# Kernel optimization log

Hardware: AMD Instinct MI355X
Metric: run time of the kernel (lower is better)

The kernel has to match this reference:

```python
import jax, jax.numpy as jnp
import numpy as np


def setup_inputs() -> dict:
    key = jax.random.key(0)
    ks = jax.random.split(key, 4)
    b, n, d, dp = 8, 4096, 256, 512
    X = jax.random.normal(ks[0], (b, n, d), dtype=jnp.float32)
    P = jax.random.normal(ks[1], (b, n, d), dtype=jnp.float32)
    # linear hypernetwork params (Kaiming-ish scale)
    Wh1 = jax.random.normal(ks[2], (d, dp), dtype=jnp.float32) * (1.0 / np.sqrt(d))
    Wh2 = jax.random.normal(ks[3], (d, dp), dtype=jnp.float32) * (1.0 / np.sqrt(d))
    bh1 = jnp.zeros((dp,), dtype=jnp.float32)
    bh2 = jnp.zeros((dp,), dtype=jnp.float32)
    return {"X": X, "P": P, "Wh1": Wh1, "bh1": bh1, "Wh2": Wh2, "bh2": bh2}


def reference(X, P, Wh1, bh1, Wh2, bh2):
    # X, P: [b, n, d]
    Xp = X + P
    # hypernetwork-generated per-sample mixing weights: [b, n, d_prime]
    W1 = Xp @ Wh1 + bh1
    W2 = Xp @ Wh2 + bh2
    # token mixing: project tokens down to d_prime "mixing" space, GELU, back up
    Pm = jnp.einsum('bnp,bnd->bpd', W1, Xp)           # [b, d_prime, d]
    A = jax.nn.gelu(Pm, approximate=False)             # torch nn.GELU is exact erf form
    Y = jnp.einsum('bnp,bpd->bnd', W2, A)              # [b, n, d]
    return Y
```

## Files before the change

kernel.cpp:

```cpp
#include <hip/hip_runtime.h>

#define DEV static __device__ __forceinline__

typedef unsigned short u16;
typedef __bf16 bf16_t;
typedef __bf16 bf16x8 __attribute__((ext_vector_type(8)));
typedef float f32x4 __attribute__((ext_vector_type(4)));
typedef u16 u16x8 __attribute__((ext_vector_type(8)));

static constexpr int Bb = 8;
static constexpr int Nn = 4096;
static constexpr int Dd = 256;
static constexpr int DP = 512;

DEV void gload16(const void* g, void* l) {
  __builtin_amdgcn_global_load_lds(
      (__attribute__((address_space(1))) void*)(unsigned long long)(g),
      (__attribute__((address_space(3))) void*)(unsigned)(unsigned long long)(l),
      16, 0, 0);
}

DEV u16 f2bf(float x) { bf16_t h = (bf16_t)x; return __builtin_bit_cast(u16, h); }
DEV float bf2f(u16 v) { unsigned u = ((unsigned)v) << 16; return __builtin_bit_cast(float, u); }
DEV float gelu_exact(float x) { return 0.5f * x * (1.0f + erff(x * 0.70710678118654752f)); }

template <int NT>
DEV void gemm_tile(const u16* Ag, int lda, const u16* Bg, int ldb,
                   int k0, int ksteps, u16* ldsA, u16* ldsB, f32x4 acc[4][NT]) {
  constexpr int BCH  = NT / 2;
  constexpr int ABUF = 4096;
  constexpr int BBUF = NT * 1024;
  const int tid  = threadIdx.x;
  const int wave = tid >> 6, lane = tid & 63;
  const int wr = wave >> 1, wc = wave & 1;
  const int lr = lane & 15, lk = (lane >> 4) * 8;
  const int srow = lane >> 2;
  const int skb  = (lane & 3) * 8;
  const int ca0 = wave * 2, ca1 = ca0 + 1;
  const size_t ga0 = (size_t)(ca0 * 16 + srow) * lda + skb;
  const size_t ga1 = (size_t)(ca1 * 16 + srow) * lda + skb;
  u16* la0 = ldsA + ca0 * 512; u16* la1 = ldsA + ca1 * 512;
  size_t gb[BCH]; u16* lb[BCH];
#pragma unroll
  for (int i = 0; i < BCH; ++i) {
    const int ch = wave * BCH + i;
    gb[i] = (size_t)(ch * 16 + srow) * ldb + skb;
    lb[i] = ldsB + ch * 512;
  }

  auto STAGE = [&](int kt, int buf) {
    const int kk = k0 + kt * 32;
    gload16(Ag + ga0 + kk, la0 + buf * ABUF);
    gload16(Ag + ga1 + kk, la1 + buf * ABUF);
#pragma unroll
    for (int i = 0; i < BCH; ++i) gload16(Bg + gb[i] + kk, lb[i] + buf * BBUF);
  };

  STAGE(0, 0);
  STAGE(1, 1);
  if constexpr (NT == 2) asm volatile("s_waitcnt vmcnt(3)" ::: "memory");
  else                   asm volatile("s_waitcnt vmcnt(4)" ::: "memory");
  __builtin_amdgcn_s_barrier();
  __builtin_amdgcn_sched_barrier(0);

  int cur = 0;
  for (int kt = 0; kt < ksteps; ++kt) {
    const int sb = (cur + 2 >= 3) ? cur - 1 : cur + 2;
    const bool do_stage = (kt + 2 < ksteps);
    if (do_stage) STAGE(kt + 2, sb);
    const u16* pa = ldsA + cur * ABUF;
    const u16* pb = ldsB + cur * BBUF;
    bf16x8 af[4], bfr[NT];
#pragma unroll
    for (int m = 0; m < 4; ++m)
      af[m] = *(const bf16x8*)(pa + (wr * 64 + m * 16 + lr) * 32 + lk);
#pragma unroll
    for (int n = 0; n < NT; ++n)
      bfr[n] = *(const bf16x8*)(pb + (wc * (NT * 16) + n * 16 + lr) * 32 + lk);
#pragma unroll
    for (int m = 0; m < 4; ++m)
#pragma unroll
      for (int n = 0; n < NT; ++n)
        acc[m][n] = __builtin_amdgcn_mfma_f32_16x16x32_bf16(af[m], bfr[n], acc[m][n], 0, 0, 0);
    if (kt + 1 < ksteps) {
      if (do_stage) {
        if constexpr (NT == 2) asm volatile("s_waitcnt vmcnt(3)" ::: "memory");
        else                   asm volatile("s_waitcnt vmcnt(4)" ::: "memory");
      } else {
        asm volatile("s_waitcnt vmcnt(0)" ::: "memory");
      }
      __builtin_amdgcn_s_barrier();
      __builtin_amdgcn_sched_barrier(0);
    }
    cur = (cur + 1 == 3) ? 0 : cur + 1;
  }
  __builtin_amdgcn_s_barrier();
}

template <int NT>
DEV void acc_zero(f32x4 acc[4][NT]) {
#pragma unroll
  for (int m = 0; m < 4; ++m)
#pragma unroll
    for (int n = 0; n < NT; ++n) {
      f32x4 z = {0.f, 0.f, 0.f, 0.f};
      acc[m][n] = z;
    }
}

__global__ __launch_bounds__(256) void k_s1(const float* __restrict__ X, const float* __restrict__ P,
                                            const float* __restrict__ Wh1, const float* __restrict__ Wh2,
                                            u16* __restrict__ Xp, u16* __restrict__ XpT,
                                            float* __restrict__ s_part,
                                            u16* __restrict__ WhT1, u16* __restrict__ Wbf2) {
  __shared__ u16 lt[64 * 65];
  const int bid = blockIdx.x;
  const int t = threadIdx.x;
  if (bid < 2048) {
    const int b  = bid >> 8;
    const int nt = (bid >> 2) & 63;
    const int dt = bid & 3;
    const int n0 = nt * 64, d0 = dt * 64;
    const int r = t >> 2, c0 = (t & 3) * 16;
    const size_t gbase = ((size_t)(b * Nn + n0 + r)) * Dd + d0 + c0;
    u16x8 lo, hi;
#pragma unroll
    for (int i = 0; i < 4; ++i) {
      float4 xv = *(const float4*)(X + gbase + i * 4);
      float4 pv = *(const float4*)(P + gbase + i * 4);
      u16 a0 = f2bf(xv.x + pv.x), a1 = f2bf(xv.y + pv.y);
      u16 a2 = f2bf(xv.z + pv.z), a3 = f2bf(xv.w + pv.w);
      if (i < 2) { lo[i*4+0]=a0; lo[i*4+1]=a1; lo[i*4+2]=a2; lo[i*4+3]=a3; }
      else       { int q=(i-2)*4; hi[q+0]=a0; hi[q+1]=a1; hi[q+2]=a2; hi[q+3]=a3; }
      lt[r * 65 + c0 + i*4 + 0] = a0; lt[r * 65 + c0 + i*4 + 1] = a1;
      lt[r * 65 + c0 + i*4 + 2] = a2; lt[r * 65 + c0 + i*4 + 3] = a3;
    }
    *(u16x8*)(Xp + gbase)     = lo;
    *(u16x8*)(Xp + gbase + 8) = hi;
    __syncthreads();
    const int dd = t >> 2, nc0 = (t & 3) * 16;
    u16x8 olo, ohi;
    float colsum = 0.f;
#pragma unroll
    for (int i = 0; i < 8; ++i) { olo[i] = lt[(nc0 + i) * 65 + dd]; colsum += bf2f(olo[i]); }
#pragma unroll
    for (int i = 0; i < 8; ++i) { ohi[i] = lt[(nc0 + 8 + i) * 65 + dd]; colsum += bf2f(ohi[i]); }
    const size_t obase = ((size_t)(b * Dd + d0 + dd)) * Nn + n0 + nc0;
    *(u16x8*)(XpT + obase)     = olo;
    *(u16x8*)(XpT + obase + 8) = ohi;
    colsum += __shfl_xor(colsum, 1);
    colsum += __shfl_xor(colsum, 2);
    if ((t & 3) == 0) s_part[(size_t)(b * 64 + nt) * Dd + d0 + dd] = colsum;
  } else if (bid < 2048 + 32) {
    const int wb = bid - 2048;
    const int rt = (wb >> 3) & 3;
    const int ct = wb & 7;
    const int r0 = rt * 64, c0t = ct * 64;
    const int r = t >> 2, c0 = (t & 3) * 16;
    const size_t gbase = (size_t)(r0 + r) * DP + c0t + c0;
#pragma unroll
    for (int i = 0; i < 4; ++i) {
      float4 v = *(const float4*)(Wh1 + gbase + i * 4);
      lt[r * 65 + c0 + i*4 + 0] = f2bf(v.x); lt[r * 65 + c0 + i*4 + 1] = f2bf(v.y);
      lt[r * 65 + c0 + i*4 + 2] = f2bf(v.z); lt[r * 65 + c0 + i*4 + 3] = f2bf(v.w);
    }
    __syncthreads();
    const int pp = t >> 2, dc0 = (t & 3) * 16;
    u16x8 olo, ohi;
#pragma unroll
    for (int i = 0; i < 8; ++i) olo[i] = lt[(dc0 + i) * 65 + pp];
#pragma unroll
    for (int i = 0; i < 8; ++i) ohi[i] = lt[(dc0 + 8 + i) * 65 + pp];
    u16* out = WhT1 + (size_t)(c0t + pp) * Dd + r0 + dc0;
    *(u16x8*)(out)     = olo;
    *(u16x8*)(out + 8) = ohi;
  } else {
    const int idx = ((bid - 2048 - 32) * 256 + t) * 8;
    float4 v0 = *(const float4*)(Wh2 + idx);
    float4 v1 = *(const float4*)(Wh2 + idx + 4);
    u16x8 o;
    o[0]=f2bf(v0.x); o[1]=f2bf(v0.y); o[2]=f2bf(v0.z); o[3]=f2bf(v0.w);
    o[4]=f2bf(v1.x); o[5]=f2bf(v1.y); o[6]=f2bf(v1.z); o[7]=f2bf(v1.w);
    *(u16x8*)(Wbf2 + idx) = o;
  }
}

__global__ __launch_bounds__(256) void k_gram(const u16* __restrict__ XpT, u16* __restrict__ G_part) {
  __shared__ __align__(16) u16 ldsA[3 * 128 * 32];
  __shared__ __align__(16) u16 ldsB[3 * 64 * 32];
  const int bid0 = blockIdx.x;
  const int bid = (bid0 & 7) * 64 + (bid0 >> 3);
  const int kc = bid & 7;
  const int tn = (bid >> 3) & 3;
  const int tm = (bid >> 5) & 1;
  const int b  = bid >> 6;
  const u16* Ag = XpT + (size_t)(b * Dd + tm * 128) * Nn;
  const u16* Bg = XpT + (size_t)(b * Dd + tn * 64) * Nn;
  f32x4 acc[4][2];
  acc_zero<2>(acc);
  gemm_tile<2>(Ag, Nn, Bg, Nn, kc * 512, 16, ldsA, ldsB, acc);
  const int tid = threadIdx.x, wave = tid >> 6, lane = tid & 63;
  const int wr = wave >> 1, wc = wave & 1, lr = lane & 15, lq = lane >> 4;
  u16* base = G_part + (size_t)kc * (Bb * Dd * Dd) + (size_t)(b * Dd + tm * 128) * Dd + tn * 64;
#pragma unroll
  for (int m = 0; m < 4; ++m)
#pragma unroll
    for (int n = 0; n < 2; ++n)
#pragma unroll
      for (int j = 0; j < 4; ++j)
        base[(size_t)(wr * 64 + m * 16 + lq * 4 + j) * Dd + wc * 32 + n * 16 + lr] =
            f2bf(acc[m][n][j]);
}

__global__ __launch_bounds__(256) void k_gsum(const u16* __restrict__ G_part,
                                              const float* __restrict__ s_part,
                                              u16* __restrict__ Gb, float* __restrict__ s,
                                              float* __restrict__ c) {
  const int bid = blockIdx.x;
  const int t = threadIdx.x;
  if (bid < 8) {
    const int b = bid, d = t;
    float sum = 0.f;
#pragma unroll 8
    for (int nt = 0; nt < 64; ++nt) sum += s_part[(size_t)(b * 64 + nt) * Dd + d];
    s[b * Dd + d] = sum;
    c[b * Dd + d] = 0.f;
  } else {
    const int e = ((bid - 8) * 256 + t) * 8;
    float a[8] = {0.f,0.f,0.f,0.f,0.f,0.f,0.f,0.f};
#pragma unroll
    for (int k = 0; k < 8; ++k) {
      u16x8 v = *(const u16x8*)(G_part + (size_t)k * (Bb * Dd * Dd) + e);
#pragma unroll
      for (int i = 0; i < 8; ++i) a[i] += bf2f(v[i]);
    }
    u16x8 o;
#pragma unroll
    for (int i = 0; i < 8; ++i) o[i] = f2bf(a[i]);
    *(u16x8*)(Gb + e) = o;
  }
}

__global__ __launch_bounds__(256) void k_pmAT(const u16* __restrict__ WhT1, const u16* __restrict__ Gb,
                                              const float* __restrict__ bh1, const float* __restrict__ s,
                                              const float* __restrict__ bh2,
                                              u16* __restrict__ AT, float* __restrict__ c) {
  __shared__ __align__(16) u16 smem[24576];
  u16* ldsA = smem;
  u16* ldsB = smem + 12288;
  u16* ct   = smem;
  const int bid = blockIdx.x;
  const int tn = bid & 1;
  const int tm = (bid >> 1) & 3;
  const int b  = bid >> 3;
  const int p0 = tm * 128, d0 = tn * 128;
  const u16* Ag = WhT1 + (size_t)p0 * Dd;
  const u16* Bg = Gb + (size_t)(b * Dd + d0) * Dd;
  f32x4 acc[4][4];
  acc_zero<4>(acc);
  gemm_tile<4>(Ag, Dd, Bg, Dd, 0, Dd / 32, ldsA, ldsB, acc);
  const int tid = threadIdx.x, wave = tid >> 6, lane = tid & 63;
  const int wr = wave >> 1, wc = wave & 1, lr = lane & 15, lq = lane >> 4;
#pragma unroll
  for (int n = 0; n < 4; ++n) {
    const int col = wc * 64 + n * 16 + lr;
    const float sv = s[b * Dd + d0 + col];
#pragma unroll
    for (int m = 0; m < 4; ++m) {
#pragma unroll
      for (int j = 0; j < 4; ++j) {
        const int row = wr * 64 + m * 16 + lq * 4 + j;
        const float pm = acc[m][n][j] + bh1[p0 + row] * sv;
        ct[col * 136 + row] = f2bf(gelu_exact(pm));
      }
    }
  }
  __syncthreads();
#pragma unroll
  for (int it = 0; it < 8; ++it) {
    const int id = tid + it * 256;
    const int dl = id >> 4, ch = id & 15;
    *(u16x8*)(AT + (size_t)(b * Dd + d0 + dl) * DP + p0 + ch * 8) =
        *(const u16x8*)(ct + dl * 136 + ch * 8);
  }
  const int ccol = tid >> 1;
  const int chalf = tid & 1;
  float csum = 0.f;
#pragma unroll
  for (int q = 0; q < 8; ++q) {
    u16x8 av = *(const u16x8*)(ct + ccol * 136 + chalf * 64 + q * 8);
#pragma unroll
    for (int i = 0; i < 8; ++i) csum += bh2[p0 + chalf * 64 + q * 8 + i] * bf2f(av[i]);
  }
  csum += __shfl_xor(csum, 1);
  if (chalf == 0) atomicAdd(c + b * Dd + d0 + ccol, csum);
}

__global__ __launch_bounds__(256) void k_h(const u16* __restrict__ Wbf2, const u16* __restrict__ AT,
                                           u16* __restrict__ HT) {
  __shared__ __align__(16) u16 smem[24576];
  u16* ldsA = smem;
  u16* ldsB = smem + 12288;
  u16* ct   = smem;
  const int bid = blockIdx.x;
  const int tn = bid & 1;
  const int tm = (bid >> 1) & 1;
  const int b  = bid >> 2;
  const int k0 = tm * 128, d0 = tn * 128;
  const u16* Ag = Wbf2 + (size_t)k0 * DP;
  const u16* Bg = AT + (size_t)(b * Dd + d0) * DP;
  f32x4 acc[4][4];
  acc_zero<4>(acc);
  gemm_tile<4>(Ag, DP, Bg, DP, 0, DP / 32, ldsA, ldsB, acc);
  const int tid = threadIdx.x, wave = tid >> 6, lane = tid & 63;
  const int wr = wave >> 1, wc = wave & 1, lr = lane & 15, lq = lane >> 4;
#pragma unroll
  for (int n = 0; n < 4; ++n) {
    const int col = wc * 64 + n * 16 + lr;
#pragma unroll
    for (int m = 0; m < 4; ++m)
#pragma unroll
      for (int j = 0; j < 4; ++j)
        ct[col * 136 + wr * 64 + m * 16 + lq * 4 + j] = f2bf(acc[m][n][j]);
  }
  __syncthreads();
#pragma unroll
  for (int it = 0; it < 8; ++it) {
    const int id = tid + it * 256;
    const int dl = id >> 4, ch = id & 15;
    *(u16x8*)(HT + (size_t)(b * Dd + d0 + dl) * Dd + k0 + ch * 8) =
        *(const u16x8*)(ct + dl * 136 + ch * 8);
  }
}

__global__ __launch_bounds__(256) void k_y(const u16* __restrict__ Xp, const u16* __restrict__ HT,
                                           const float* __restrict__ c, float* __restrict__ Y) {
  __shared__ __align__(16) u16 ldsA[3 * 128 * 32];
  __shared__ __align__(16) u16 ldsB[3 * 64 * 32];
  const int bid0 = blockIdx.x;
  const int bid = (bid0 & 7) * 128 + (bid0 >> 3);
  const int b  = bid >> 7;
  const int tm = (bid >> 2) & 31;
  const int tn = bid & 3;
  const u16* Ag = Xp + (size_t)(b * Nn + tm * 128) * Dd;
  const u16* Bg = HT + (size_t)(b * Dd + tn * 64) * Dd;
  f32x4 acc[4][2];
  acc_zero<2>(acc);
  gemm_tile<2>(Ag, Dd, Bg, Dd, 0, Dd / 32, ldsA, ldsB, acc);
  const int tid = threadIdx.x, wave = tid >> 6, lane = tid & 63;
  const int wr = wave >> 1, wc = wave & 1, lr = lane & 15, lq = lane >> 4;
  float* base = Y + (size_t)(b * Nn + tm * 128) * Dd + tn * 64;
#pragma unroll
  for (int n = 0; n < 2; ++n) {
    const int col = wc * 32 + n * 16 + lr;
    const float cv = c[b * Dd + tn * 64 + col];
#pragma unroll
    for (int m = 0; m < 4; ++m)
#pragma unroll
      for (int j = 0; j < 4; ++j)
        base[(size_t)(wr * 64 + m * 16 + lq * 4 + j) * Dd + col] = acc[m][n][j] + cv;
  }
}

extern "C" void kernel_launch(void* const* d_in, const int* in_sizes, int n_in,
                              void* d_out, int out_size, void* d_ws, size_t ws_size,
                              hipStream_t stream) {
  const float* X   = (const float*)d_in[0];
  const float* P   = (const float*)d_in[1];
  const float* Wh1 = (const float*)d_in[2];
  const float* bh1 = (const float*)d_in[3];
  const float* Wh2 = (const float*)d_in[4];
  const float* bh2 = (const float*)d_in[5];
  float* Y = (float*)d_out;
  char* ws = (char*)d_ws;

  u16*   Xp     = (u16*)(ws);
  u16*   XpT    = (u16*)(ws + 16777216);
  u16*   WhT1   = (u16*)(ws + 33554432);
  u16*   Wbf2   = (u16*)(ws + 33816576);
  u16*   G_part = (u16*)(ws + 34078720);
  float* s_part = (float*)(ws + 42467328);
  float* s      = (float*)(ws + 42991616);
  float* c      = (float*)(ws + 42999808);
  u16*   Gb     = (u16*)(ws + 43008000);
  u16*   AT     = (u16*)(ws + 44056576);
  u16*   HT     = (u16*)(ws + 46153728);
  const size_t WS_NEED = 47202304;
  if (ws_size < WS_NEED) return;

  k_s1  <<<2144, 256, 0, stream>>>(X, P, Wh1, Wh2, Xp, XpT, s_part, WhT1, Wbf2);
  k_gram<<<512,  256, 0, stream>>>(XpT, G_part);
  k_gsum<<<264,  256, 0, stream>>>(G_part, s_part, Gb, s, c);
  k_pmAT<<<64,   256, 0, stream>>>(WhT1, Gb, bh1, s, bh2, AT, c);
  k_h   <<<32,   256, 0, stream>>>(Wbf2, AT, HT);
  k_y   <<<1024, 256, 0, stream>>>(Xp, HT, c, Y);
}
```

Baseline: 68.00 us.

## Fuse gram reduction, Pm/GELU, and H GEMM into one kernel with grid counter

Removes the separate k_gsum, k_pmAT and k_h launches. The split-K gram partials are now summed while loading the B operand of the Pm GEMM, and the H GEMM runs in the first 32 blocks once a global atomic counter shows all 64 blocks have written AT. The c bias is written as per-tile partials and summed in k_y, so the atomics on c and the zeroing of c are no longer needed. This saves launch gaps and a round trip through memory, but it relies on all 64 blocks being resident at once for the spin-wait, and the Pm loop now has only two LDS buffers with no prefetch overlap.

```diff
diff --git a/kernel.cpp b/kernel.cpp
--- a/kernel.cpp
+++ b/kernel.cpp
@@ -185,10 +185,12 @@
   }
 }
 
-__global__ __launch_bounds__(256) void k_gram(const u16* __restrict__ XpT, u16* __restrict__ G_part) {
+__global__ __launch_bounds__(256) void k_gram(const u16* __restrict__ XpT, u16* __restrict__ G_part,
+                                              int* __restrict__ ctr) {
   __shared__ __align__(16) u16 ldsA[3 * 128 * 32];
   __shared__ __align__(16) u16 ldsB[3 * 64 * 32];
   const int bid0 = blockIdx.x;
+  if (bid0 == 512) { if (threadIdx.x == 0) *ctr = 0; return; }
   const int bid = (bid0 & 7) * 64 + (bid0 >> 3);
   const int kc = bid & 7;
   const int tn = (bid >> 3) & 3;
@@ -212,129 +214,161 @@
             f2bf(acc[m][n][j]);
 }
 
-__global__ __launch_bounds__(256) void k_gsum(const u16* __restrict__ G_part,
-                                              const float* __restrict__ s_part,
-                                              u16* __restrict__ Gb, float* __restrict__ s,
-                                              float* __restrict__ c) {
+__global__ __launch_bounds__(256) void k_pmATh(
+    const u16* __restrict__ WhT1, const u16* __restrict__ G_part,
+    const float* __restrict__ s_part, const float* __restrict__ bh1,
+    const float* __restrict__ bh2, const u16* __restrict__ Wbf2,
+    u16* __restrict__ AT, float* __restrict__ c_part, u16* __restrict__ HT,
+    int* __restrict__ ctr) {
+  __shared__ __align__(16) u16 smem[24576];
+  __shared__ float sv[128];
   const int bid = blockIdx.x;
-  const int t = threadIdx.x;
-  if (bid < 8) {
-    const int b = bid, d = t;
-    float sum = 0.f;
+  const int tid = threadIdx.x;
+  const int wave = tid >> 6, lane = tid & 63;
+  const int wr = wave >> 1, wc = wave & 1, lr = lane & 15, lq = lane >> 4;
+  const int lk = lq * 8;
+
+  {
+    const int tnb = bid & 1;
+    const int tmb = (bid >> 1) & 3;
+    const int bb  = bid >> 3;
+    const int p0 = tmb * 128, d0 = tnb * 128;
+
+    if (tid < 128) {
+      float sum = 0.f;
 #pragma unroll 8
-    for (int nt = 0; nt < 64; ++nt) sum += s_part[(size_t)(b * 64 + nt) * Dd + d];
-    s[b * Dd + d] = sum;
-    c[b * Dd + d] = 0.f;
-  } else {
-    const int e = ((bid - 8) * 256 + t) * 8;
-    float a[8] = {0.f,0.f,0.f,0.f,0.f,0.f,0.f,0.f};
-#pragma unroll
-    for (int k = 0; k < 8; ++k) {
-      u16x8 v = *(const u16x8*)(G_part + (size_t)k * (Bb * Dd * Dd) + e);
-#pragma unroll
-      for (int i = 0; i < 8; ++i) a[i] += bf2f(v[i]);
-    }
-    u16x8 o;
-#pragma unroll
-    for (int i = 0; i < 8; ++i) o[i] = f2bf(a[i]);
-    *(u16x8*)(Gb + e) = o;
-  }
-}
-
-__global__ __launch_bounds__(256) void k_pmAT(const u16* __restrict__ WhT1, const u16* __restrict__ Gb,
-                                              const float* __restrict__ bh1, const float* __restrict__ s,
-                                              const float* __restrict__ bh2,
-                                              u16* __restrict__ AT, float* __restrict__ c) {
-  __shared__ __align__(16) u16 smem[24576];
-  u16* ldsA = smem;
-  u16* ldsB = smem + 12288;
-  u16* ct   = smem;
-  const int bid = blockIdx.x;
-  const int tn = bid & 1;
-  const int tm = (bid >> 1) & 3;
-  const int b  = bid >> 3;
-  const int p0 = tm * 128, d0 = tn * 128;
-  const u16* Ag = WhT1 + (size_t)p0 * Dd;
-  const u16* Bg = Gb + (size_t)(b * Dd + d0) * Dd;
-  f32x4 acc[4][4];
-  acc_zero<4>(acc);
-  gemm_tile<4>(Ag, Dd, Bg, Dd, 0, Dd / 32, ldsA, ldsB, acc);
-  const int tid = threadIdx.x, wave = tid >> 6, lane = tid & 63;
-  const int wr = wave >> 1, wc = wave & 1, lr = lane & 15, lq = lane >> 4;
-#pragma unroll
-  for (int n = 0; n < 4; ++n) {
-    const int col = wc * 64 + n * 16 + lr;
-    const float sv = s[b * Dd + d0 + col];
-#pragma unroll
-    for (int m = 0; m < 4; ++m) {
-#pragma unroll
-      for (int j = 0; j < 4; ++j) {
-        const int row = wr * 64 + m * 16 + lq * 4 + j;
-        const float pm = acc[m][n][j] + bh1[p0 + row] * sv;
-        ct[col * 136 + row] = f2bf(gelu_exact(pm));
+      for (int nt = 0; nt < 64; ++nt) sum += s_part[(size_t)(bb * 64 + nt) * Dd + d0 + tid];
+      sv[tid] = sum;
+    }
+
+    const u16* Ag = WhT1 + (size_t)p0 * Dd;
+    const int srow = lane >> 2, skb = (lane & 3) * 8;
+    const int ca0 = wave * 2, ca1 = ca0 + 1;
+    const size_t ga0 = (size_t)(ca0 * 16 + srow) * Dd + skb;
+    const size_t ga1 = (size_t)(ca1 * 16 + srow) * Dd + skb;
+    const int brow = tid >> 1, bhalf = tid & 1;
+    const u16* Bbase = G_part + (size_t)(bb * Dd + d0 + brow) * Dd + bhalf * 16;
+
+    f32x4 acc[4][4];
+    acc_zero<4>(acc);
+    for (int kt = 0; kt < 8; ++kt) {
+      const int buf = kt & 1;
+      u16* lA = smem + buf * 4096;
+      u16* lB = smem + 8192 + buf * 4096;
+      gload16(Ag + ga0 + kt * 32, lA + ca0 * 512);
+      gload16(Ag + ga1 + kt * 32, lA + ca1 * 512);
+      float a[16];
+#pragma unroll
+      for (int i = 0; i < 16; ++i) a[i] = 0.f;
+#pragma unroll
+      for (int sl = 0; sl < 8; ++sl) {
+        const u16* p = Bbase + (size_t)sl * (Bb * Dd * Dd) + kt * 32;
+        u16x8 v0 = *(const u16x8*)p;
+        u16x8 v1 = *(const u16x8*)(p + 8);
+#pragma unroll
+        for (int i = 0; i < 8; ++i) { a[i] += bf2f(v0[i]); a[8 + i] += bf2f(v1[i]); }
       }
-    }
-  }
+      u16x8 o0, o1;
+#pragma unroll
+      for (int i = 0; i < 8; ++i) { o0[i] = f2bf(a[i]); o1[i] = f2bf(a[8 + i]); }
+      *(u16x8*)(lB + brow * 32 + bhalf * 16)     = o0;
+      *(u16x8*)(lB + brow * 32 + bhalf * 16 + 8) = o1;
+      asm volatile("s_waitcnt vmcnt(0)" ::: "memory");
+      __syncthreads();
+      bf16x8 af[4], bfr[4];
+#pragma unroll
+      for (int m = 0; m < 4; ++m)
+        af[m] = *(const bf16x8*)(lA + (wr * 64 + m * 16 + lr) * 32 + lk);
+#pragma unroll
+      for (int n = 0; n < 4; ++n)
+        bfr[n] = *(const bf16x8*)(lB + (wc * 64 + n * 16 + lr) * 32 + lk);
+#pragma unroll
+      for (int m = 0; m < 4; ++m)
+#pragma unroll
+        for (int n = 0; n < 4; ++n)
+          acc[m][n] = __builtin_amdgcn_mfma_f32_16x16x32_bf16(af[m], bfr[n], acc[m][n], 0, 0, 0);
+      __syncthreads();
+    }
+
+    u16* ct = smem;
+#pragma unroll
+    for (int n = 0; n < 4; ++n) {
+      const int col = wc * 64 + n * 16 + lr;
+      const float svv = sv[col];
+#pragma unroll
+      for (int m = 0; m < 4; ++m) {
+#pragma unroll
+        for (int j = 0; j < 4; ++j) {
+          const int row = wr * 64 + m * 16 + lq * 4 + j;
+          const float pm = acc[m][n][j] + bh1[p0 + row] * svv;
+          ct[col * 136 + row] = f2bf(gelu_exact(pm));
+        }
+      }
+    }
+    __syncthreads();
+#pragma unroll
+    for (int it = 0; it < 8; ++it) {
+      const int id = tid + it * 256;
+      const int dl = id >> 4, ch = id & 15;
+      *(u16x8*)(AT + (size_t)(bb * Dd + d0 + dl) * DP + p0 + ch * 8) =
+          *(const u16x8*)(ct + dl * 136 + ch * 8);
+    }
+    const int ccol = tid >> 1;
+    const int chalf = tid & 1;
+    float csum = 0.f;
+#pragma unroll
+    for (int q = 0; q < 8; ++q) {
+      u16x8 av = *(const u16x8*)(ct + ccol * 136 + chalf * 64 + q * 8);
+#pragma unroll
+      for (int i = 0; i < 8; ++i) csum += bh2[p0 + chalf * 64 + q * 8 + i] * bf2f(av[i]);
+    }
+    csum += __shfl_xor(csum, 1);
+    if (chalf == 0) c_part[(size_t)(bb * 4 + tmb) * Dd + d0 + ccol] = csum;
+  }
+
+  __threadfence();
   __syncthreads();
-#pragma unroll
-  for (int it = 0; it < 8; ++it) {
-    const int id = tid + it * 256;
-    const int dl = id >> 4, ch = id & 15;
-    *(u16x8*)(AT + (size_t)(b * Dd + d0 + dl) * DP + p0 + ch * 8) =
-        *(const u16x8*)(ct + dl * 136 + ch * 8);
-  }
-  const int ccol = tid >> 1;
-  const int chalf = tid & 1;
-  float csum = 0.f;
-#pragma unroll
-  for (int q = 0; q < 8; ++q) {
-    u16x8 av = *(const u16x8*)(ct + ccol * 136 + chalf * 64 + q * 8);
-#pragma unroll
-    for (int i = 0; i < 8; ++i) csum += bh2[p0 + chalf * 64 + q * 8 + i] * bf2f(av[i]);
-  }
-  csum += __shfl_xor(csum, 1);
-  if (chalf == 0) atomicAdd(c + b * Dd + d0 + ccol, csum);
-}
-
-__global__ __launch_bounds__(256) void k_h(const u16* __restrict__ Wbf2, const u16* __restrict__ AT,
-                                           u16* __restrict__ HT) {
-  __shared__ __align__(16) u16 smem[24576];
-  u16* ldsA = smem;
-  u16* ldsB = smem + 12288;
-  u16* ct   = smem;
-  const int bid = blockIdx.x;
-  const int tn = bid & 1;
-  const int tm = (bid >> 1) & 1;
-  const int b  = bid >> 2;
-  const int k0 = tm * 128, d0 = tn * 128;
-  const u16* Ag = Wbf2 + (size_t)k0 * DP;
-  const u16* Bg = AT + (size_t)(b * Dd + d0) * DP;
-  f32x4 acc[4][4];
-  acc_zero<4>(acc);
-  gemm_tile<4>(Ag, DP, Bg, DP, 0, DP / 32, ldsA, ldsB, acc);
-  const int tid = threadIdx.x, wave = tid >> 6, lane = tid & 63;
-  const int wr = wave >> 1, wc = wave & 1, lr = lane & 15, lq = lane >> 4;
-#pragma unroll
-  for (int n = 0; n < 4; ++n) {
-    const int col = wc * 64 + n * 16 + lr;
-#pragma unroll
-    for (int m = 0; m < 4; ++m)
-#pragma unroll
-      for (int j = 0; j < 4; ++j)
-        ct[col * 136 + wr * 64 + m * 16 + lq * 4 + j] = f2bf(acc[m][n][j]);
+  if (tid == 0) atomicAdd(ctr, 1);
+  if (bid >= 32) return;
+  if (tid == 0) {
+    while (atomicAdd(ctr, 0) < 64) __builtin_amdgcn_s_sleep(8);
   }
   __syncthreads();
-#pragma unroll
-  for (int it = 0; it < 8; ++it) {
-    const int id = tid + it * 256;
-    const int dl = id >> 4, ch = id & 15;
-    *(u16x8*)(HT + (size_t)(b * Dd + d0 + dl) * Dd + k0 + ch * 8) =
-        *(const u16x8*)(ct + dl * 136 + ch * 8);
+  __threadfence();
+
+  {
+    const int tn = bid & 1;
+    const int tm = (bid >> 1) & 1;
+    const int b  = bid >> 2;
+    const int k0 = tm * 128, d0 = tn * 128;
+    const u16* Ag = Wbf2 + (size_t)k0 * DP;
+    const u16* Bg = AT + (size_t)(b * Dd + d0) * DP;
+    f32x4 acc[4][4];
+    acc_zero<4>(acc);
+    gemm_tile<4>(Ag, DP, Bg, DP, 0, DP / 32, smem, smem + 12288, acc);
+    u16* ct = smem;
+#pragma unroll
+    for (int n = 0; n < 4; ++n) {
+      const int col = wc * 64 + n * 16 + lr;
+#pragma unroll
+      for (int m = 0; m < 4; ++m)
+#pragma unroll
+        for (int j = 0; j < 4; ++j)
+          ct[col * 136 + wr * 64 + m * 16 + lq * 4 + j] = f2bf(acc[m][n][j]);
+    }
+    __syncthreads();
+#pragma unroll
+    for (int it = 0; it < 8; ++it) {
+      const int id = tid + it * 256;
+      const int dl = id >> 4, ch = id & 15;
+      *(u16x8*)(HT + (size_t)(b * Dd + d0 + dl) * Dd + k0 + ch * 8) =
+          *(const u16x8*)(ct + dl * 136 + ch * 8);
+    }
   }
 }
 
 __global__ __launch_bounds__(256) void k_y(const u16* __restrict__ Xp, const u16* __restrict__ HT,
-                                           const float* __restrict__ c, float* __restrict__ Y) {
+                                           const float* __restrict__ c_part, float* __restrict__ Y) {
   __shared__ __align__(16) u16 ldsA[3 * 128 * 32];
   __shared__ __align__(16) u16 ldsB[3 * 64 * 32];
   const int bid0 = blockIdx.x;
@@ -353,7 +387,9 @@
 #pragma unroll
   for (int n = 0; n < 2; ++n) {
     const int col = wc * 32 + n * 16 + lr;
-    const float cv = c[b * Dd + tn * 64 + col];
+    const int gcol = tn * 64 + col;
+    float cv = c_part[(size_t)(b * 4 + 0) * Dd + gcol] + c_part[(size_t)(b * 4 + 1) * Dd + gcol]
+             + c_part[(size_t)(b * 4 + 2) * Dd + gcol] + c_part[(size_t)(b * 4 + 3) * Dd + gcol];
 #pragma unroll
     for (int m = 0; m < 4; ++m)
 #pragma unroll
@@ -380,18 +416,15 @@
   u16*   Wbf2   = (u16*)(ws + 33816576);
   u16*   G_part = (u16*)(ws + 34078720);
   float* s_part = (float*)(ws + 42467328);
-  float* s      = (float*)(ws + 42991616);
-  float* c      = (float*)(ws + 42999808);
-  u16*   Gb     = (u16*)(ws + 43008000);
-  u16*   AT     = (u16*)(ws + 44056576);
-  u16*   HT     = (u16*)(ws + 46153728);
-  const size_t WS_NEED = 47202304;
+  float* c_part = (float*)(ws + 42991616);
+  int*   ctr    = (int*)(ws + 43024384);
+  u16*   AT     = (u16*)(ws + 43024512);
+  u16*   HT     = (u16*)(ws + 45121664);
+  const size_t WS_NEED = 46170240;
   if (ws_size < WS_NEED) return;
 
-  k_s1  <<<2144, 256, 0, stream>>>(X, P, Wh1, Wh2, Xp, XpT, s_part, WhT1, Wbf2);
-  k_gram<<<512,  256, 0, stream>>>(XpT, G_part);
-  k_gsum<<<264,  256, 0, stream>>>(G_part, s_part, Gb, s, c);
-  k_pmAT<<<64,   256, 0, stream>>>(WhT1, Gb, bh1, s, bh2, AT, c);
-  k_h   <<<32,   256, 0, stream>>>(Wbf2, AT, HT);
-  k_y   <<<1024, 256, 0, stream>>>(Xp, HT, c, Y);
-}
+  k_s1   <<<2144, 256, 0, stream>>>(X, P, Wh1, Wh2, Xp, XpT, s_part, WhT1, Wbf2);
+  k_gram <<<513,  256, 0, stream>>>(XpT, G_part, ctr);
+  k_pmATh<<<64,   256, 0, stream>>>(WhT1, G_part, s_part, bh1, bh2, Wbf2, AT, c_part, HT, ctr);
+  k_y    <<<1024, 256, 0, stream>>>(Xp, HT, c_part, Y);
+}
```

After: 85.29 us. 25.4% more time.

## Fuse GELU mixing-matrix kernel with H projection, keeping activations in LDS

Applied to the files above, without the earlier changes.

Merges k_pmAT and k_h into one kernel. Each block loops over the four d_prime tiles, computes the GELU activation tile into shared memory, and immediately accumulates the Wh2 product into registers. This removes the AT round-trip through global memory, one kernel launch, and the atomic accumulation of c, since c is now written directly. In exchange the grid shrinks from 64 to 32 blocks, the first GEMM is recomputed by both km blocks, and the inner H loop is serialized with synchronous loads and no prefetch.

```diff
diff --git a/kernel.cpp b/kernel.cpp
--- a/kernel.cpp
+++ b/kernel.cpp
@@ -214,8 +214,7 @@
 
 __global__ __launch_bounds__(256) void k_gsum(const u16* __restrict__ G_part,
                                               const float* __restrict__ s_part,
-                                              u16* __restrict__ Gb, float* __restrict__ s,
-                                              float* __restrict__ c) {
+                                              u16* __restrict__ Gb, float* __restrict__ s) {
   const int bid = blockIdx.x;
   const int t = threadIdx.x;
   if (bid < 8) {
@@ -224,7 +223,6 @@
 #pragma unroll 8
     for (int nt = 0; nt < 64; ++nt) sum += s_part[(size_t)(b * 64 + nt) * Dd + d];
     s[b * Dd + d] = sum;
-    c[b * Dd + d] = 0.f;
   } else {
     const int e = ((bid - 8) * 256 + t) * 8;
     float a[8] = {0.f,0.f,0.f,0.f,0.f,0.f,0.f,0.f};
@@ -241,87 +239,95 @@
   }
 }
 
-__global__ __launch_bounds__(256) void k_pmAT(const u16* __restrict__ WhT1, const u16* __restrict__ Gb,
-                                              const float* __restrict__ bh1, const float* __restrict__ s,
-                                              const float* __restrict__ bh2,
-                                              u16* __restrict__ AT, float* __restrict__ c) {
+__global__ __launch_bounds__(256) void k_pmATh(
+    const u16* __restrict__ WhT1, const u16* __restrict__ Gb,
+    const float* __restrict__ bh1, const float* __restrict__ s,
+    const float* __restrict__ bh2, const u16* __restrict__ Wbf2,
+    float* __restrict__ c, u16* __restrict__ HT) {
   __shared__ __align__(16) u16 smem[24576];
   u16* ldsA = smem;
   u16* ldsB = smem + 12288;
-  u16* ct   = smem;
+  u16* act  = smem;
+  u16* hA   = smem + 17920;
   const int bid = blockIdx.x;
-  const int tn = bid & 1;
-  const int tm = (bid >> 1) & 3;
-  const int b  = bid >> 3;
-  const int p0 = tm * 128, d0 = tn * 128;
-  const u16* Ag = WhT1 + (size_t)p0 * Dd;
-  const u16* Bg = Gb + (size_t)(b * Dd + d0) * Dd;
-  f32x4 acc[4][4];
-  acc_zero<4>(acc);
-  gemm_tile<4>(Ag, Dd, Bg, Dd, 0, Dd / 32, ldsA, ldsB, acc);
-  const int tid = threadIdx.x, wave = tid >> 6, lane = tid & 63;
+  const int km = bid & 1;
+  const int tn = (bid >> 1) & 1;
+  const int b  = bid >> 2;
+  const int d0 = tn * 128, k0 = km * 128;
+  const int tid = threadIdx.x;
+  const int wave = tid >> 6, lane = tid & 63;
   const int wr = wave >> 1, wc = wave & 1, lr = lane & 15, lq = lane >> 4;
+  const int lk = lq * 8;
+  const int srow = lane >> 2, skb = (lane & 3) * 8;
+  const int ca0 = wave * 2, ca1 = ca0 + 1;
+  const int ccol = tid >> 1, chalf = tid & 1;
+
+  f32x4 acch[4][4];
+  acc_zero<4>(acch);
+  float csum = 0.f;
+
+  for (int tm = 0; tm < 4; ++tm) {
+    const int p0 = tm * 128;
+    f32x4 accA[4][4];
+    acc_zero<4>(accA);
+    gemm_tile<4>(WhT1 + (size_t)p0 * Dd, Dd, Gb + (size_t)(b * Dd + d0) * Dd, Dd,
+                 0, Dd / 32, ldsA, ldsB, accA);
+#pragma unroll
+    for (int n = 0; n < 4; ++n) {
+      const int col = wc * 64 + n * 16 + lr;
+      const float sv = s[b * Dd + d0 + col];
+#pragma unroll
+      for (int m = 0; m < 4; ++m)
+#pragma unroll
+        for (int j = 0; j < 4; ++j) {
+          const int row = wr * 64 + m * 16 + lq * 4 + j;
+          act[col * 136 + row] = f2bf(gelu_exact(accA[m][n][j] + bh1[p0 + row] * sv));
+        }
+    }
+    __syncthreads();
+    if (km == 0) {
+#pragma unroll
+      for (int q = 0; q < 8; ++q) {
+        u16x8 av = *(const u16x8*)(act + ccol * 136 + chalf * 64 + q * 8);
+#pragma unroll
+        for (int i = 0; i < 8; ++i) csum += bh2[p0 + chalf * 64 + q * 8 + i] * bf2f(av[i]);
+      }
+    }
+    for (int kt = 0; kt < 4; ++kt) {
+      gload16(Wbf2 + (size_t)(k0 + ca0 * 16 + srow) * DP + p0 + kt * 32 + skb, hA + ca0 * 512);
+      gload16(Wbf2 + (size_t)(k0 + ca1 * 16 + srow) * DP + p0 + kt * 32 + skb, hA + ca1 * 512);
+      asm volatile("s_waitcnt vmcnt(0)" ::: "memory");
+      __syncthreads();
+      bf16x8 af[4], bfr[4];
+#pragma unroll
+      for (int m = 0; m < 4; ++m)
+        af[m] = *(const bf16x8*)(hA + (wr * 64 + m * 16 + lr) * 32 + lk);
+#pragma unroll
+      for (int n = 0; n < 4; ++n)
+        bfr[n] = *(const bf16x8*)(act + (wc * 64 + n * 16 + lr) * 136 + kt * 32 + lk);
+#pragma unroll
+      for (int m = 0; m < 4; ++m)
+#pragma unroll
+        for (int n = 0; n < 4; ++n)
+          acch[m][n] = __builtin_amdgcn_mfma_f32_16x16x32_bf16(af[m], bfr[n], acch[m][n], 0, 0, 0);
+      __syncthreads();
+    }
+  }
+
+  if (km == 0) {
+    csum += __shfl_xor(csum, 1);
+    if (chalf == 0) c[b * Dd + d0 + ccol] = csum;
+  }
+
+  u16* ct = smem;
 #pragma unroll
   for (int n = 0; n < 4; ++n) {
     const int col = wc * 64 + n * 16 + lr;
-    const float sv = s[b * Dd + d0 + col];
-#pragma unroll
-    for (int m = 0; m < 4; ++m) {
-#pragma unroll
-      for (int j = 0; j < 4; ++j) {
-        const int row = wr * 64 + m * 16 + lq * 4 + j;
-        const float pm = acc[m][n][j] + bh1[p0 + row] * sv;
-        ct[col * 136 + row] = f2bf(gelu_exact(pm));
-      }
-    }
-  }
-  __syncthreads();
-#pragma unroll
-  for (int it = 0; it < 8; ++it) {
-    const int id = tid + it * 256;
-    const int dl = id >> 4, ch = id & 15;
-    *(u16x8*)(AT + (size_t)(b * Dd + d0 + dl) * DP + p0 + ch * 8) =
-        *(const u16x8*)(ct + dl * 136 + ch * 8);
-  }
-  const int ccol = tid >> 1;
-  const int chalf = tid & 1;
-  float csum = 0.f;
-#pragma unroll
-  for (int q = 0; q < 8; ++q) {
-    u16x8 av = *(const u16x8*)(ct + ccol * 136 + chalf * 64 + q * 8);
-#pragma unroll
-    for (int i = 0; i < 8; ++i) csum += bh2[p0 + chalf * 64 + q * 8 + i] * bf2f(av[i]);
-  }
-  csum += __shfl_xor(csum, 1);
-  if (chalf == 0) atomicAdd(c + b * Dd + d0 + ccol, csum);
-}
-
-__global__ __launch_bounds__(256) void k_h(const u16* __restrict__ Wbf2, const u16* __restrict__ AT,
-                                           u16* __restrict__ HT) {
-  __shared__ __align__(16) u16 smem[24576];
-  u16* ldsA = smem;
-  u16* ldsB = smem + 12288;
-  u16* ct   = smem;
-  const int bid = blockIdx.x;
-  const int tn = bid & 1;
-  const int tm = (bid >> 1) & 1;
-  const int b  = bid >> 2;
-  const int k0 = tm * 128, d0 = tn * 128;
-  const u16* Ag = Wbf2 + (size_t)k0 * DP;
-  const u16* Bg = AT + (size_t)(b * Dd + d0) * DP;
-  f32x4 acc[4][4];
-  acc_zero<4>(acc);
-  gemm_tile<4>(Ag, DP, Bg, DP, 0, DP / 32, ldsA, ldsB, acc);
-  const int tid = threadIdx.x, wave = tid >> 6, lane = tid & 63;
-  const int wr = wave >> 1, wc = wave & 1, lr = lane & 15, lq = lane >> 4;
-#pragma unroll
-  for (int n = 0; n < 4; ++n) {
-    const int col = wc * 64 + n * 16 + lr;
 #pragma unroll
     for (int m = 0; m < 4; ++m)
 #pragma unroll
       for (int j = 0; j < 4; ++j)
-        ct[col * 136 + wr * 64 + m * 16 + lq * 4 + j] = f2bf(acc[m][n][j]);
+        ct[col * 136 + wr * 64 + m * 16 + lq * 4 + j] = f2bf(acch[m][n][j]);
   }
   __syncthreads();
 #pragma unroll
@@ -383,15 +389,13 @@
   float* s      = (float*)(ws + 42991616);
   float* c      = (float*)(ws + 42999808);
   u16*   Gb     = (u16*)(ws + 43008000);
-  u16*   AT     = (u16*)(ws + 44056576);
-  u16*   HT     = (u16*)(ws + 46153728);
-  const size_t WS_NEED = 47202304;
+  u16*   HT     = (u16*)(ws + 44056576);
+  const size_t WS_NEED = 45105152;
   if (ws_size < WS_NEED) return;
 
-  k_s1  <<<2144, 256, 0, stream>>>(X, P, Wh1, Wh2, Xp, XpT, s_part, WhT1, Wbf2);
-  k_gram<<<512,  256, 0, stream>>>(XpT, G_part);
-  k_gsum<<<264,  256, 0, stream>>>(G_part, s_part, Gb, s, c);
-  k_pmAT<<<64,   256, 0, stream>>>(WhT1, Gb, bh1, s, bh2, AT, c);
-  k_h   <<<32,   256, 0, stream>>>(Wbf2, AT, HT);
-  k_y   <<<1024, 256, 0, stream>>>(Xp, HT, c, Y);
-}
+  k_s1   <<<2144, 256, 0, stream>>>(X, P, Wh1, Wh2, Xp, XpT, s_part, WhT1, Wbf2);
+  k_gram <<<512,  256, 0, stream>>>(XpT, G_part);
+  k_gsum <<<264,  256, 0, stream>>>(G_part, s_part, Gb, s);
+  k_pmATh<<<32,   256, 0, stream>>>(WhT1, Gb, bh1, s, bh2, Wbf2, c, HT);
+  k_y    <<<1024, 256, 0, stream>>>(Xp, HT, c, Y);
+}
```

Result: slower. 101.4 us (+49.2%).

## Fuse split-K gram reduction into k_gram via last-block counters; halve pmAT/h tiles

Applied to the files above, without the earlier changes.

Removes the separate k_gsum launch. Each split-K gram tile group now bumps an atomic counter, and the last of its 8 blocks sums the bf16 partials into Gb. The s reduction moves into k_pmAT, and the atomic c accumulation becomes per-tile c_part partials that k_y sums. k_pmAT and k_h switch to 128x64 tiles, doubling their grid sizes to raise parallelism in those small stages. This saves one launch and adds fence/atomic overhead plus a serialized tail reduction in the last block of each group.

```diff
diff --git a/kernel.cpp b/kernel.cpp
--- a/kernel.cpp
+++ b/kernel.cpp
@@ -112,7 +112,8 @@
                                             const float* __restrict__ Wh1, const float* __restrict__ Wh2,
                                             u16* __restrict__ Xp, u16* __restrict__ XpT,
                                             float* __restrict__ s_part,
-                                            u16* __restrict__ WhT1, u16* __restrict__ Wbf2) {
+                                            u16* __restrict__ WhT1, u16* __restrict__ Wbf2,
+                                            int* __restrict__ ctr) {
   __shared__ u16 lt[64 * 65];
   const int bid = blockIdx.x;
   const int t = threadIdx.x;
@@ -174,7 +175,7 @@
     u16* out = WhT1 + (size_t)(c0t + pp) * Dd + r0 + dc0;
     *(u16x8*)(out)     = olo;
     *(u16x8*)(out + 8) = ohi;
-  } else {
+  } else if (bid < 2048 + 32 + 64) {
     const int idx = ((bid - 2048 - 32) * 256 + t) * 8;
     float4 v0 = *(const float4*)(Wh2 + idx);
     float4 v1 = *(const float4*)(Wh2 + idx + 4);
@@ -182,12 +183,16 @@
     o[0]=f2bf(v0.x); o[1]=f2bf(v0.y); o[2]=f2bf(v0.z); o[3]=f2bf(v0.w);
     o[4]=f2bf(v1.x); o[5]=f2bf(v1.y); o[6]=f2bf(v1.z); o[7]=f2bf(v1.w);
     *(u16x8*)(Wbf2 + idx) = o;
-  }
-}
-
-__global__ __launch_bounds__(256) void k_gram(const u16* __restrict__ XpT, u16* __restrict__ G_part) {
+  } else {
+    if (t < 64) ctr[t] = 0;
+  }
+}
+
+__global__ __launch_bounds__(256) void k_gram(const u16* __restrict__ XpT, u16* __restrict__ G_part,
+                                              u16* __restrict__ Gb, int* __restrict__ ctr) {
   __shared__ __align__(16) u16 ldsA[3 * 128 * 32];
   __shared__ __align__(16) u16 ldsB[3 * 64 * 32];
+  __shared__ int lastFlag;
   const int bid0 = blockIdx.x;
   const int bid = (bid0 & 7) * 64 + (bid0 >> 3);
   const int kc = bid & 7;
@@ -210,113 +215,118 @@
       for (int j = 0; j < 4; ++j)
         base[(size_t)(wr * 64 + m * 16 + lq * 4 + j) * Dd + wc * 32 + n * 16 + lr] =
             f2bf(acc[m][n][j]);
-}
-
-__global__ __launch_bounds__(256) void k_gsum(const u16* __restrict__ G_part,
+
+  __threadfence();
+  __syncthreads();
+  const int group = (b * 2 + tm) * 4 + tn;
+  if (tid == 0) lastFlag = (atomicAdd(&ctr[group], 1) == 7);
+  __syncthreads();
+  if (!lastFlag) return;
+  __threadfence();
+
+  const int r = tid >> 1, hf = tid & 1;
+  const size_t off = (size_t)(b * Dd + tm * 128 + r) * Dd + tn * 64 + hf * 32;
+  float a[32];
+#pragma unroll
+  for (int i = 0; i < 32; ++i) a[i] = 0.f;
+  for (int k = 0; k < 8; ++k) {
+    const u16* p = G_part + (size_t)k * (Bb * Dd * Dd) + off;
+#pragma unroll
+    for (int ch = 0; ch < 4; ++ch) {
+      u16x8 v = *(const u16x8*)(p + ch * 8);
+#pragma unroll
+      for (int i = 0; i < 8; ++i) a[ch * 8 + i] += bf2f(v[i]);
+    }
+  }
+#pragma unroll
+  for (int ch = 0; ch < 4; ++ch) {
+    u16x8 o;
+#pragma unroll
+    for (int i = 0; i < 8; ++i) o[i] = f2bf(a[ch * 8 + i]);
+    *(u16x8*)(Gb + off + ch * 8) = o;
+  }
+}
+
+__global__ __launch_bounds__(256) void k_pmAT(const u16* __restrict__ WhT1, const u16* __restrict__ Gb,
                                               const float* __restrict__ s_part,
-                                              u16* __restrict__ Gb, float* __restrict__ s,
-                                              float* __restrict__ c) {
+                                              const float* __restrict__ bh1, const float* __restrict__ bh2,
+                                              u16* __restrict__ AT, float* __restrict__ c_part) {
+  __shared__ __align__(16) u16 smem[18432];
+  __shared__ float sv[64];
   const int bid = blockIdx.x;
-  const int t = threadIdx.x;
-  if (bid < 8) {
-    const int b = bid, d = t;
+  const int tn = bid & 3;
+  const int tm = (bid >> 2) & 3;
+  const int b  = bid >> 4;
+  const int p0 = tm * 128, d0 = tn * 64;
+  const int tid = threadIdx.x;
+  if (tid < 64) {
     float sum = 0.f;
 #pragma unroll 8
-    for (int nt = 0; nt < 64; ++nt) sum += s_part[(size_t)(b * 64 + nt) * Dd + d];
-    s[b * Dd + d] = sum;
-    c[b * Dd + d] = 0.f;
-  } else {
-    const int e = ((bid - 8) * 256 + t) * 8;
-    float a[8] = {0.f,0.f,0.f,0.f,0.f,0.f,0.f,0.f};
-#pragma unroll
-    for (int k = 0; k < 8; ++k) {
-      u16x8 v = *(const u16x8*)(G_part + (size_t)k * (Bb * Dd * Dd) + e);
-#pragma unroll
-      for (int i = 0; i < 8; ++i) a[i] += bf2f(v[i]);
-    }
-    u16x8 o;
-#pragma unroll
-    for (int i = 0; i < 8; ++i) o[i] = f2bf(a[i]);
-    *(u16x8*)(Gb + e) = o;
-  }
-}
-
-__global__ __launch_bounds__(256) void k_pmAT(const u16* __restrict__ WhT1, const u16* __restrict__ Gb,
-                                              const float* __restrict__ bh1, const float* __restrict__ s,
-                                              const float* __restrict__ bh2,
-                                              u16* __restrict__ AT, float* __restrict__ c) {
-  __shared__ __align__(16) u16 smem[24576];
+    for (int nt = 0; nt < 64; ++nt) sum += s_part[(size_t)(b * 64 + nt) * Dd + d0 + tid];
+    sv[tid] = sum;
+  }
+  u16* ldsA = smem;
+  u16* ldsB = smem + 12288;
+  f32x4 acc[4][2];
+  acc_zero<2>(acc);
+  gemm_tile<2>(WhT1 + (size_t)p0 * Dd, Dd, Gb + (size_t)(b * Dd + d0) * Dd, Dd,
+               0, Dd / 32, ldsA, ldsB, acc);
+  const int wave = tid >> 6, lane = tid & 63;
+  const int wr = wave >> 1, wc = wave & 1, lr = lane & 15, lq = lane >> 4;
+  u16* ct = smem;
+#pragma unroll
+  for (int n = 0; n < 2; ++n) {
+    const int col = wc * 32 + n * 16 + lr;
+    const float svv = sv[col];
+#pragma unroll
+    for (int m = 0; m < 4; ++m)
+#pragma unroll
+      for (int j = 0; j < 4; ++j) {
+        const int row = wr * 64 + m * 16 + lq * 4 + j;
+        ct[col * 136 + row] = f2bf(gelu_exact(acc[m][n][j] + bh1[p0 + row] * svv));
+      }
+  }
+  __syncthreads();
+#pragma unroll
+  for (int it = 0; it < 4; ++it) {
+    const int id = tid + it * 256;
+    const int dl = id >> 4, ch = id & 15;
+    *(u16x8*)(AT + (size_t)(b * Dd + d0 + dl) * DP + p0 + ch * 8) =
+        *(const u16x8*)(ct + dl * 136 + ch * 8);
+  }
+  const int ccol = tid >> 2, qtr = tid & 3;
+  float csum = 0.f;
+#pragma unroll
+  for (int q = 0; q < 4; ++q) {
+    u16x8 av = *(const u16x8*)(ct + ccol * 136 + qtr * 32 + q * 8);
+#pragma unroll
+    for (int i = 0; i < 8; ++i) csum += bh2[p0 + qtr * 32 + q * 8 + i] * bf2f(av[i]);
+  }
+  csum += __shfl_xor(csum, 1);
+  csum += __shfl_xor(csum, 2);
+  if (qtr == 0) c_part[(size_t)(b * 4 + tm) * Dd + d0 + ccol] = csum;
+}
+
+__global__ __launch_bounds__(256) void k_h(const u16* __restrict__ Wbf2, const u16* __restrict__ AT,
+                                           u16* __restrict__ HT) {
+  __shared__ __align__(16) u16 smem[18432];
   u16* ldsA = smem;
   u16* ldsB = smem + 12288;
   u16* ct   = smem;
   const int bid = blockIdx.x;
-  const int tn = bid & 1;
-  const int tm = (bid >> 1) & 3;
+  const int tn = bid & 3;
+  const int tm = (bid >> 2) & 1;
   const int b  = bid >> 3;
-  const int p0 = tm * 128, d0 = tn * 128;
-  const u16* Ag = WhT1 + (size_t)p0 * Dd;
-  const u16* Bg = Gb + (size_t)(b * Dd + d0) * Dd;
-  f32x4 acc[4][4];
-  acc_zero<4>(acc);
-  gemm_tile<4>(Ag, Dd, Bg, Dd, 0, Dd / 32, ldsA, ldsB, acc);
+  const int k0 = tm * 128, d0 = tn * 64;
+  f32x4 acc[4][2];
+  acc_zero<2>(acc);
+  gemm_tile<2>(Wbf2 + (size_t)k0 * DP, DP, AT + (size_t)(b * Dd + d0) * DP, DP,
+               0, DP / 32, ldsA, ldsB, acc);
   const int tid = threadIdx.x, wave = tid >> 6, lane = tid & 63;
   const int wr = wave >> 1, wc = wave & 1, lr = lane & 15, lq = lane >> 4;
 #pragma unroll
-  for (int n = 0; n < 4; ++n) {
-    const int col = wc * 64 + n * 16 + lr;
-    const float sv = s[b * Dd + d0 + col];
-#pragma unroll
-    for (int m = 0; m < 4; ++m) {
-#pragma unroll
-      for (int j = 0; j < 4; ++j) {
-        const int row = wr * 64 + m * 16 + lq * 4 + j;
-        const float pm = acc[m][n][j] + bh1[p0 + row] * sv;
-        ct[col * 136 + row] = f2bf(gelu_exact(pm));
-      }
-    }
-  }
-  __syncthreads();
-#pragma unroll
-  for (int it = 0; it < 8; ++it) {
-    const int id = tid + it * 256;
-    const int dl = id >> 4, ch = id & 15;
-    *(u16x8*)(AT + (size_t)(b * Dd + d0 + dl) * DP + p0 + ch * 8) =
-        *(const u16x8*)(ct + dl * 136 + ch * 8);
-  }
-  const int ccol = tid >> 1;
-  const int chalf = tid & 1;
-  float csum = 0.f;
-#pragma unroll
-  for (int q = 0; q < 8; ++q) {
-    u16x8 av = *(const u16x8*)(ct + ccol * 136 + chalf * 64 + q * 8);
-#pragma unroll
-    for (int i = 0; i < 8; ++i) csum += bh2[p0 + chalf * 64 + q * 8 + i] * bf2f(av[i]);
-  }
-  csum += __shfl_xor(csum, 1);
-  if (chalf == 0) atomicAdd(c + b * Dd + d0 + ccol, csum);
-}
-
-__global__ __launch_bounds__(256) void k_h(const u16* __restrict__ Wbf2, const u16* __restrict__ AT,
-                                           u16* __restrict__ HT) {
-  __shared__ __align__(16) u16 smem[24576];
-  u16* ldsA = smem;
-  u16* ldsB = smem + 12288;
-  u16* ct   = smem;
-  const int bid = blockIdx.x;
-  const int tn = bid & 1;
-  const int tm = (bid >> 1) & 1;
-  const int b  = bid >> 2;
-  const int k0 = tm * 128, d0 = tn * 128;
-  const u16* Ag = Wbf2 + (size_t)k0 * DP;
-  const u16* Bg = AT + (size_t)(b * Dd + d0) * DP;
-  f32x4 acc[4][4];
-  acc_zero<4>(acc);
-  gemm_tile<4>(Ag, DP, Bg, DP, 0, DP / 32, ldsA, ldsB, acc);
-  const int tid = threadIdx.x, wave = tid >> 6, lane = tid & 63;
-  const int wr = wave >> 1, wc = wave & 1, lr = lane & 15, lq = lane >> 4;
-#pragma unroll
-  for (int n = 0; n < 4; ++n) {
-    const int col = wc * 64 + n * 16 + lr;
+  for (int n = 0; n < 2; ++n) {
+    const int col = wc * 32 + n * 16 + lr;
 #pragma unroll
     for (int m = 0; m < 4; ++m)
 #pragma unroll
@@ -325,7 +335,7 @@
   }
   __syncthreads();
 #pragma unroll
-  for (int it = 0; it < 8; ++it) {
+  for (int it = 0; it < 4; ++it) {
     const int id = tid + it * 256;
     const int dl = id >> 4, ch = id & 15;
     *(u16x8*)(HT + (size_t)(b * Dd + d0 + dl) * Dd + k0 + ch * 8) =
@@ -334,7 +344,7 @@
 }
 
 __global__ __launch_bounds__(256) void k_y(const u16* __restrict__ Xp, const u16* __restrict__ HT,
-                                           const float* __restrict__ c, float* __restrict__ Y) {
+                                           const float* __restrict__ c_part, float* __restrict__ Y) {
   __shared__ __align__(16) u16 ldsA[3 * 128 * 32];
   __shared__ __align__(16) u16 ldsB[3 * 64 * 32];
   const int bid0 = blockIdx.x;
@@ -353,7 +363,9 @@
 #pragma unroll
   for (int n = 0; n < 2; ++n) {
     const int col = wc * 32 + n * 16 + lr;
-    const float cv = c[b * Dd + tn * 64 + col];
+    const int gcol = tn * 64 + col;
+    const float cv = c_part[(size_t)(b * 4 + 0) * Dd + gcol] + c_part[(size_t)(b * 4 + 1) * Dd + gcol]
+                   + c_part[(size_t)(b * 4 + 2) * Dd + gcol] + c_part[(size_t)(b * 4 + 3) * Dd + gcol];
 #pragma unroll
     for (int m = 0; m < 4; ++m)
 #pragma unroll
@@ -380,18 +392,17 @@
   u16*   Wbf2   = (u16*)(ws + 33816576);
   u16*   G_part = (u16*)(ws + 34078720);
   float* s_part = (float*)(ws + 42467328);
-  float* s      = (float*)(ws + 42991616);
-  float* c      = (float*)(ws + 42999808);
-  u16*   Gb     = (u16*)(ws + 43008000);
-  u16*   AT     = (u16*)(ws + 44056576);
-  u16*   HT     = (u16*)(ws + 46153728);
-  const size_t WS_NEED = 47202304;
+  float* c_part = (float*)(ws + 42991616);
+  int*   ctr    = (int*)(ws + 43024384);
+  u16*   Gb     = (u16*)(ws + 43024640);
+  u16*   AT     = (u16*)(ws + 44073216);
+  u16*   HT     = (u16*)(ws + 46170368);
+  const size_t WS_NEED = 47218944;
   if (ws_size < WS_NEED) return;
 
-  k_s1  <<<2144, 256, 0, stream>>>(X, P, Wh1, Wh2, Xp, XpT, s_part, WhT1, Wbf2);
-  k_gram<<<512,  256, 0, stream>>>(XpT, G_part);
-  k_gsum<<<264,  256, 0, stream>>>(G_part, s_part, Gb, s, c);
-  k_pmAT<<<64,   256, 0, stream>>>(WhT1, Gb, bh1, s, bh2, AT, c);
-  k_h   <<<32,   256, 0, stream>>>(Wbf2, AT, HT);
-  k_y   <<<1024, 256, 0, stream>>>(Xp, HT, c, Y);
-}
+  k_s1  <<<2145, 256, 0, stream>>>(X, P, Wh1, Wh2, Xp, XpT, s_part, WhT1, Wbf2, ctr);
+  k_gram<<<512,  256, 0, stream>>>(XpT, G_part, Gb, ctr);
+  k_pmAT<<<128,  256, 0, stream>>>(WhT1, Gb, s_part, bh1, bh2, AT, c_part);
+  k_h   <<<64,   256, 0, stream>>>(Wbf2, AT, HT);
+  k_y   <<<1024, 256, 0, stream>>>(Xp, HT, c_part, Y);
+}
```

New measurement: 135.2 us. 98.8% more time.
